# Optimization experiments

Measured on AMD Instinct MI355X. Metric: run time of the kernel, lower is better.

The kernel has to match this reference:

```python
import math
import jax, jax.numpy as jnp
import numpy as np

N_EMBD = 256
N_HEAD = 4
MLP_MULT = 64
N = MLP_MULT * N_EMBD // N_HEAD  # 4096, head feature dim
THETA = 2 ** 16
B, T = 2, 2048


def get_freqs(n: int, theta: int) -> jnp.ndarray:
    # quantize arange to multiples of 2 (pairs share a frequency)
    idx = jnp.arange(n, dtype=jnp.float32)
    q = jnp.floor(idx / 2.0) * 2.0
    return 1.0 / theta ** (q / n) / (2.0 * math.pi)


def _rope(phases: jnp.ndarray, v: jnp.ndarray) -> jnp.ndarray:
    # interleaved rotation: (-v_odd, v_even) re-interleaved
    v_rot = jnp.stack((-v[..., 1::2], v[..., ::2]), axis=-1).reshape(v.shape)
    ph = (phases % 1.0) * (2.0 * math.pi)
    return v * jnp.cos(ph) + v_rot * jnp.sin(ph)


def setup_inputs() -> dict:
    key = jax.random.key(0)
    kq, kk, kv = jax.random.split(key, 3)
    Q = jax.random.normal(kq, (B, N_HEAD, T, N), dtype=jnp.float32)
    K = jax.random.normal(kk, (B, N_HEAD, T, N), dtype=jnp.float32)
    V = jax.random.normal(kv, (B, N_HEAD, T, N), dtype=jnp.float32)
    return {"Q": Q, "K": K, "V": V}


def reference(Q, K, V):
    t = Q.shape[2]
    freqs = get_freqs(N, THETA)  # [N]
    # phases: [1,1,T,N]
    r_phases = jnp.arange(t, dtype=jnp.float32)[None, None, :, None] * freqs[None, None, None, :]
    Q32 = Q.astype(jnp.float32)
    V32 = V.astype(jnp.float32)
    QR = _rope(r_phases, Q32)  # [B,nh,T,N]
    scale = 1.0 / math.sqrt(N)
    scores = jnp.einsum('bhtn,bhsn->bhts', QR, QR) * scale  # [B,nh,T,T], no softmax
    out = jnp.einsum('bhts,bhsn->bhtn', scores, V32)
    return out.astype(Q.dtype)
```

## Files before the change

### kernel.cpp

```cpp
#include <hip/hip_runtime.h>
#include <stdint.h>

#define B_  2
#define H_  4
#define T_  2048
#define N_  4096
#define BH  8

#define BM 256
#define BN 256
#define BK 64

typedef __attribute__((ext_vector_type(8))) short  short8;
typedef __attribute__((ext_vector_type(4))) float  floatx4;


__device__ __forceinline__ unsigned short f2bf(float x) {
  union { float f; unsigned u; } un; un.f = x;
  unsigned r = un.u + 0x7FFFu + ((un.u >> 16) & 1u);
  return (unsigned short)(r >> 16);
}

__device__ __forceinline__ void async_copy16(const void* g, void* l) {
  __builtin_amdgcn_global_load_lds(
      (const __attribute__((address_space(1))) unsigned int*)g,
      (__attribute__((address_space(3))) unsigned int*)l,
      16, 0, 0);
}

__global__ __launch_bounds__(256)
void rope_cast_kernel(const float* __restrict__ Q, unsigned short* __restrict__ QR) {
  const long e0 = ((long)blockIdx.x * 256 + threadIdx.x) * 8;
  const float4 v0 = *(const float4*)(Q + e0);
  const float4 v1 = *(const float4*)(Q + e0 + 4);
  const int   n0 = (int)(e0 & (N_ - 1));
  const float t  = (float)((int)((e0 >> 12) & (T_ - 1)));
  float vv[8] = {v0.x, v0.y, v0.z, v0.w, v1.x, v1.y, v1.z, v1.w};
  union { short8 v; unsigned short u[8]; } o;
#pragma unroll
  for (int p = 0; p < 4; ++p) {
    const int n = n0 + 2 * p;
    const float freq = exp2f(-(float)n * (1.0f / 256.0f)) * 0.15915494309189535f;
    const float ph = t * freq;
    const float fr = ph - floorf(ph);
    const float s = __builtin_amdgcn_sinf(fr);
    const float c = __builtin_amdgcn_cosf(fr);
    o.u[2 * p]     = f2bf(vv[2 * p] * c - vv[2 * p + 1] * s);
    o.u[2 * p + 1] = f2bf(vv[2 * p + 1] * c + vv[2 * p] * s);
  }
  *(short8*)(QR + e0) = o.v;
}

__global__ __launch_bounds__(256)
void transpose_cast_kernel(const float* __restrict__ V, unsigned short* __restrict__ Vt) {
  __shared__ float tile[64][65];
  const long bh = blockIdx.z;
  const float* Vb = V + bh * (long)T_ * N_;
  unsigned short* Vtb = Vt + bh * (long)N_ * T_;
  const int s0 = blockIdx.x * 64;
  const int n0 = blockIdx.y * 64;
  const int tx = threadIdx.x & 63;
  const int ty = threadIdx.x >> 6;
#pragma unroll
  for (int i = 0; i < 16; ++i) {
    const int r = ty * 16 + i;
    tile[r][tx] = Vb[(long)(s0 + r) * N_ + n0 + tx];
  }
  __syncthreads();
#pragma unroll
  for (int i = 0; i < 16; ++i) {
    const int r = ty * 16 + i;
    Vtb[(long)(n0 + r) * T_ + s0 + tx] = f2bf(tile[tx][r]);
  }
}

__device__ __forceinline__ const short8* frag_ptr(const unsigned short* base, int row, int colel) {
  const int half = row >> 7;
  const int r    = row & 127;
  int o = r * 128 + colel * 2;
  o ^= (r & 7) << 4;
  return (const short8*)((const char*)base + half * 16384 + o);
}

__device__ __forceinline__ void load_a8(short8 a[8], const unsigned short* tp, int rb, int lr, int lk) {
#pragma unroll
  for (int f = 0; f < 4; ++f)
#pragma unroll
    for (int s = 0; s < 2; ++s)
      a[f * 2 + s] = *frag_ptr(tp, rb + f * 16 + lr, s * 32 + lk);
}

__device__ __forceinline__ void load_b4(short8 b[4], const unsigned short* tp, int rb, int lr, int lk) {
#pragma unroll
  for (int c = 0; c < 2; ++c)
#pragma unroll
    for (int s = 0; s < 2; ++s)
      b[c * 2 + s] = *frag_ptr(tp, rb + c * 16 + lr, s * 32 + lk);
}

template<int QI, int QJ>
__device__ __forceinline__ void mfma_quad(floatx4 (&acc)[8][4], const short8* a, const short8* b) {
#pragma unroll
  for (int s = 0; s < 2; ++s)
#pragma unroll
    for (int f = 0; f < 4; ++f)
#pragma unroll
      for (int c = 0; c < 2; ++c)
        acc[QI * 4 + f][QJ * 2 + c] = __builtin_amdgcn_mfma_f32_16x16x32_bf16(
            a[f * 2 + s], b[c * 2 + s], acc[QI * 4 + f][QJ * 2 + c], 0, 0, 0);
}

template <typename OutT>
__global__ __launch_bounds__(512, 2)
void gemm_bt8(const unsigned short* __restrict__ A, const unsigned short* __restrict__ B,
              OutT* __restrict__ C, int M, int Nc, int K, float alpha,
              long sA, long sB, long sC)
{
  __shared__ unsigned short smem[4][16384];

  const int nx = (int)gridDim.x, ny = (int)gridDim.y;
  const int nwg = nx * ny * (int)gridDim.z;
  const int idx = (int)blockIdx.x + nx * ((int)blockIdx.y + ny * (int)blockIdx.z);
  const int wg = ((nwg & 7) == 0) ? ((idx & 7) * (nwg >> 3) + (idx >> 3)) : idx;
  const int bx = wg % nx;
  const int by = (wg / nx) % ny;
  const int bz = wg / (nx * ny);

  const unsigned short* Ab = A + bz * sA;
  const unsigned short* Bb = B + bz * sB;
  OutT* Cb = C + bz * sC;
  const int tM = by * BM, tN = bx * BN;

  const int tid  = (int)threadIdx.x;
  const int lane = tid & 63;
  const int wave = tid >> 6;
  const int wm = wave >> 2;
  const int wn = wave & 3;
  const int lr = lane & 15;
  const int lk = (lane >> 4) * 8;

  const int sr = wave * 8 + (lane >> 3);
  const int sc = ((((lane & 7) * 16) ^ ((lane >> 3) << 4)) >> 1);
  const long aoff = (long)(tM + sr) * K + sc;
  const long boff = (long)(tN + sr) * K + sc;
  const int NT = K / BK;

  #define STAGE(Gb, off, kt, h, Lhalf) do {                                        \
    const unsigned short* _g = (Gb) + (off) + (long)(h) * 128 * K + (long)(kt) * 64; \
    async_copy16(_g,                &(Lhalf)[wave * 512]);                          \
    async_copy16(_g + (long)64 * K, &(Lhalf)[4096 + wave * 512]);                   \
  } while (0)

  STAGE(Bb, boff, 0, 0, &smem[1][0]);
  STAGE(Bb, boff, 0, 1, &smem[1][8192]);
  STAGE(Ab, aoff, 0, 0, &smem[0][0]);
  STAGE(Ab, aoff, 0, 1, &smem[0][8192]);
  const int k1 = (NT > 1) ? 1 : 0;
  STAGE(Bb, boff, k1, 0, &smem[3][0]);
  STAGE(Bb, boff, k1, 1, &smem[3][8192]);
  asm volatile("s_waitcnt vmcnt(4)" ::: "memory");
  __builtin_amdgcn_s_barrier();

  floatx4 acc[8][4] = {};
  short8 a[8], b0[4], b1[4];

  for (int t = 0; t < NT; ++t) {
    const unsigned short* Ac = smem[(t & 1) * 2 + 0];
    const unsigned short* Bc = smem[(t & 1) * 2 + 1];
    unsigned short* An = smem[((t + 1) & 1) * 2 + 0];
    unsigned short* Bn = smem[(t & 1) * 2 + 1];
    const int ktA = (t + 1 < NT) ? t + 1 : NT - 1;
    const int ktB = (t + 2 < NT) ? t + 2 : NT - 1;

    load_a8(a,  Ac, wm * 128 + 0,  lr, lk);
    load_b4(b0, Bc, wn * 64 + 0,   lr, lk);
    STAGE(Ab, aoff, ktA, 0, &An[0]);
    __builtin_amdgcn_s_barrier();
    asm volatile("s_waitcnt lgkmcnt(0)" ::: "memory");
    __builtin_amdgcn_s_setprio(1);
    mfma_quad<0, 0>(acc, a, b0);
    __builtin_amdgcn_s_setprio(0);
    __builtin_amdgcn_s_barrier();

    load_b4(b1, Bc, wn * 64 + 32, lr, lk);
    STAGE(Ab, aoff, ktA, 1, &An[8192]);
    __builtin_amdgcn_s_barrier();
    asm volatile("s_waitcnt lgkmcnt(0)" ::: "memory");
    __builtin_amdgcn_s_setprio(1);
    mfma_quad<0, 1>(acc, a, b1);
    __builtin_amdgcn_s_setprio(0);
    __builtin_amdgcn_s_barrier();

    load_a8(a, Ac, wm * 128 + 64, lr, lk);
    STAGE(Bb, boff, ktB, 0, &Bn[0]);
    __builtin_amdgcn_s_barrier();
    asm volatile("s_waitcnt lgkmcnt(0)" ::: "memory");
    __builtin_amdgcn_s_setprio(1);
    mfma_quad<1, 1>(acc, a, b1);
    __builtin_amdgcn_s_setprio(0);
    __builtin_amdgcn_s_barrier();

    STAGE(Bb, boff, ktB, 1, &Bn[8192]);
    asm volatile("s_waitcnt vmcnt(4)" ::: "memory");
    __builtin_amdgcn_s_barrier();
    __builtin_amdgcn_s_setprio(1);
    mfma_quad<1, 0>(acc, a, b0);
    __builtin_amdgcn_s_setprio(0);
    __builtin_amdgcn_s_barrier();
  }
  #undef STAGE

  const int crow = (lane >> 4) * 4;
  const int ccol = lane & 15;
#pragma unroll
  for (int f = 0; f < 8; ++f)
#pragma unroll
    for (int c = 0; c < 4; ++c)
#pragma unroll
      for (int r = 0; r < 4; ++r) {
        const long row = tM + wm * 128 + f * 16 + crow + r;
        const long col = tN + wn * 64 + c * 16 + ccol;
        const float v = acc[f][c][r] * alpha;
        OutT* p = &Cb[row * (long)Nc + col];
        if constexpr (sizeof(OutT) == 2) *p = (OutT)f2bf(v);
        else                             *p = (OutT)v;
      }
}

extern "C" void kernel_launch(void* const* d_in, const int* in_sizes, int n_in,
                              void* d_out, int out_size, void* d_ws, size_t ws_size,
                              hipStream_t stream) {
  const float* Q = (const float*)d_in[0];
  const float* V = (const float*)d_in[2];
  float* O = (float*)d_out;

  unsigned short* QRb = (unsigned short*)d_ws;
  unsigned short* Vtb = QRb + (size_t)BH * T_ * N_;
  unsigned short* S   = Vtb + (size_t)BH * T_ * N_;

  rope_cast_kernel<<<(BH * (long)T_ * N_) / (8 * 256), 256, 0, stream>>>(Q, QRb);
  transpose_cast_kernel<<<dim3(T_ / 64, N_ / 64, BH), 256, 0, stream>>>(V, Vtb);
  gemm_bt8<unsigned short><<<dim3(T_ / BN, T_ / BM, BH), 512, 0, stream>>>(
      QRb, QRb, S, T_, T_, N_, 1.0f / 64.0f,
      (long)T_ * N_, (long)T_ * N_, (long)T_ * T_);
  gemm_bt8<float><<<dim3(N_ / BN, T_ / BM, BH), 512, 0, stream>>>(
      S, Vtb, O, T_, N_, T_, 1.0f,
      (long)T_ * T_, (long)N_ * T_, (long)T_ * N_);
}
```

Before: 1.154 ms.

## Merge rope and transpose prep kernels, vectorize transpose, precompute LDS fragment addresses

Merges the RoPE-cast and V transpose-cast kernels into one launch that picks its role by block index, which removes a kernel launch and lets the two memory-bound passes share the GPU. The transpose now does float4 global reads and 16-byte bf16 writes instead of scalar accesses. The GEMM hoists the swizzled LDS fragment addresses out of the inner loop as per-lane byte offsets with parity toggling, which cuts the integer address math per iteration. Merging the kernels also makes every rope block reserve the transpose tile in shared memory, and the hand-written address math has to match the old swizzle exactly.

```diff
diff --git a/kernel.cpp b/kernel.cpp
--- a/kernel.cpp
+++ b/kernel.cpp
@@ -11,6 +11,9 @@
 #define BN 256
 #define BK 64
 
+#define ROPE_BLOCKS  ((BH * (long)T_ * N_) / (8 * 256))
+#define TRANS_BLOCKS ((T_ / 64) * (N_ / 64) * BH)
+
 typedef __attribute__((ext_vector_type(8))) short  short8;
 typedef __attribute__((ext_vector_type(4))) float  floatx4;
 
@@ -29,73 +32,62 @@
 }
 
 __global__ __launch_bounds__(256)
-void rope_cast_kernel(const float* __restrict__ Q, unsigned short* __restrict__ QR) {
-  const long e0 = ((long)blockIdx.x * 256 + threadIdx.x) * 8;
-  const float4 v0 = *(const float4*)(Q + e0);
-  const float4 v1 = *(const float4*)(Q + e0 + 4);
-  const int   n0 = (int)(e0 & (N_ - 1));
-  const float t  = (float)((int)((e0 >> 12) & (T_ - 1)));
-  float vv[8] = {v0.x, v0.y, v0.z, v0.w, v1.x, v1.y, v1.z, v1.w};
-  union { short8 v; unsigned short u[8]; } o;
-#pragma unroll
-  for (int p = 0; p < 4; ++p) {
-    const int n = n0 + 2 * p;
-    const float freq = exp2f(-(float)n * (1.0f / 256.0f)) * 0.15915494309189535f;
-    const float ph = t * freq;
-    const float fr = ph - floorf(ph);
-    const float s = __builtin_amdgcn_sinf(fr);
-    const float c = __builtin_amdgcn_cosf(fr);
-    o.u[2 * p]     = f2bf(vv[2 * p] * c - vv[2 * p + 1] * s);
-    o.u[2 * p + 1] = f2bf(vv[2 * p + 1] * c + vv[2 * p] * s);
+void prep_kernel(const float* __restrict__ Q, unsigned short* __restrict__ QR,
+                 const float* __restrict__ V, unsigned short* __restrict__ Vt) {
+  __shared__ float tile[64][65];
+  const int bid = (int)blockIdx.x;
+
+  if (bid < (int)ROPE_BLOCKS) {
+    const long e0 = ((long)bid * 256 + threadIdx.x) * 8;
+    const float4 v0 = *(const float4*)(Q + e0);
+    const float4 v1 = *(const float4*)(Q + e0 + 4);
+    const int   n0 = (int)(e0 & (N_ - 1));
+    const float t  = (float)((int)((e0 >> 12) & (T_ - 1)));
+    float vv[8] = {v0.x, v0.y, v0.z, v0.w, v1.x, v1.y, v1.z, v1.w};
+    union { short8 v; unsigned short u[8]; } o;
+#pragma unroll
+    for (int p = 0; p < 4; ++p) {
+      const int n = n0 + 2 * p;
+      const float freq = exp2f(-(float)n * (1.0f / 256.0f)) * 0.15915494309189535f;
+      const float ph = t * freq;
+      const float fr = ph - floorf(ph);
+      const float s = __builtin_amdgcn_sinf(fr);
+      const float c = __builtin_amdgcn_cosf(fr);
+      o.u[2 * p]     = f2bf(vv[2 * p] * c - vv[2 * p + 1] * s);
+      o.u[2 * p + 1] = f2bf(vv[2 * p + 1] * c + vv[2 * p] * s);
+    }
+    *(short8*)(QR + e0) = o.v;
+  } else {
+    const int tb = bid - (int)ROPE_BLOCKS;
+    const int sxi = tb & 31;
+    const int nyi = (tb >> 5) & 63;
+    const long bh = tb >> 11;
+    const float* Vb = V + bh * (long)T_ * N_;
+    unsigned short* Vtb = Vt + bh * (long)N_ * T_;
+    const int s0 = sxi * 64;
+    const int n0 = nyi * 64;
+    const int c = threadIdx.x & 15;
+    const int r = threadIdx.x >> 4;
+#pragma unroll
+    for (int i = 0; i < 4; ++i) {
+      const float4 v = *(const float4*)(Vb + (long)(s0 + r + 16 * i) * N_ + n0 + c * 4);
+      tile[r + 16 * i][c * 4 + 0] = v.x;
+      tile[r + 16 * i][c * 4 + 1] = v.y;
+      tile[r + 16 * i][c * 4 + 2] = v.z;
+      tile[r + 16 * i][c * 4 + 3] = v.w;
+    }
+    __syncthreads();
+    const int rn = threadIdx.x >> 3;
+    const int cs = threadIdx.x & 7;
+#pragma unroll
+    for (int i = 0; i < 2; ++i) {
+      const int n = rn + 32 * i;
+      union { short8 v; unsigned short u[8]; } o;
+#pragma unroll
+      for (int k = 0; k < 8; ++k) o.u[k] = f2bf(tile[cs * 8 + k][n]);
+      *(short8*)(Vtb + (long)(n0 + n) * T_ + s0 + cs * 8) = o.v;
+    }
   }
-  *(short8*)(QR + e0) = o.v;
-}
-
-__global__ __launch_bounds__(256)
-void transpose_cast_kernel(const float* __restrict__ V, unsigned short* __restrict__ Vt) {
-  __shared__ float tile[64][65];
-  const long bh = blockIdx.z;
-  const float* Vb = V + bh * (long)T_ * N_;
-  unsigned short* Vtb = Vt + bh * (long)N_ * T_;
-  const int s0 = blockIdx.x * 64;
-  const int n0 = blockIdx.y * 64;
-  const int tx = threadIdx.x & 63;
-  const int ty = threadIdx.x >> 6;
-#pragma unroll
-  for (int i = 0; i < 16; ++i) {
-    const int r = ty * 16 + i;
-    tile[r][tx] = Vb[(long)(s0 + r) * N_ + n0 + tx];
-  }
-  __syncthreads();
-#pragma unroll
-  for (int i = 0; i < 16; ++i) {
-    const int r = ty * 16 + i;
-    Vtb[(long)(n0 + r) * T_ + s0 + tx] = f2bf(tile[tx][r]);
-  }
-}
-
-__device__ __forceinline__ const short8* frag_ptr(const unsigned short* base, int row, int colel) {
-  const int half = row >> 7;
-  const int r    = row & 127;
-  int o = r * 128 + colel * 2;
-  o ^= (r & 7) << 4;
-  return (const short8*)((const char*)base + half * 16384 + o);
-}
-
-__device__ __forceinline__ void load_a8(short8 a[8], const unsigned short* tp, int rb, int lr, int lk) {
-#pragma unroll
-  for (int f = 0; f < 4; ++f)
-#pragma unroll
-    for (int s = 0; s < 2; ++s)
-      a[f * 2 + s] = *frag_ptr(tp, rb + f * 16 + lr, s * 32 + lk);
-}
-
-__device__ __forceinline__ void load_b4(short8 b[4], const unsigned short* tp, int rb, int lr, int lk) {
-#pragma unroll
-  for (int c = 0; c < 2; ++c)
-#pragma unroll
-    for (int s = 0; s < 2; ++s)
-      b[c * 2 + s] = *frag_ptr(tp, rb + c * 16 + lr, s * 32 + lk);
 }
 
 template<int QI, int QJ>
@@ -117,6 +109,7 @@
               long sA, long sB, long sC)
 {
   __shared__ unsigned short smem[4][16384];
+  char* smemb = (char*)smem;
 
   const int nx = (int)gridDim.x, ny = (int)gridDim.y;
   const int nwg = nx * ny * (int)gridDim.z;
@@ -139,25 +132,32 @@
   const int lr = lane & 15;
   const int lk = (lane >> 4) * 8;
 
+  const unsigned swz   = (unsigned)(lane & 7) << 4;
+  const unsigned lowA0 = ((unsigned)(lk * 2)     ) ^ swz;
+  const unsigned lowA1 = ((unsigned)(lk * 2) + 64) ^ swz;
+  const unsigned aB4   = (unsigned)wm * 16384u + (unsigned)lr * 128u;
+  const unsigned bB4   = 32768u + (unsigned)(wn >> 1) * 16384u
+                       + (unsigned)(wn & 1) * 8192u + (unsigned)lr * 128u;
+
   const int sr = wave * 8 + (lane >> 3);
   const int sc = ((((lane & 7) * 16) ^ ((lane >> 3) << 4)) >> 1);
-  const long aoff = (long)(tM + sr) * K + sc;
-  const long boff = (long)(tN + sr) * K + sc;
+  const unsigned short* gA = Ab + (long)(tM + sr) * K + sc;
+  const unsigned short* gB = Bb + (long)(tN + sr) * K + sc;
   const int NT = K / BK;
 
-  #define STAGE(Gb, off, kt, h, Lhalf) do {                                        \
-    const unsigned short* _g = (Gb) + (off) + (long)(h) * 128 * K + (long)(kt) * 64; \
-    async_copy16(_g,                &(Lhalf)[wave * 512]);                          \
-    async_copy16(_g + (long)64 * K, &(Lhalf)[4096 + wave * 512]);                   \
+  #define STAGE2(gbase, kt, h, ldst) do {                                          \
+    const unsigned short* _g = (gbase) + (long)(kt) * 64 + (long)((h) * 128) * K;  \
+    async_copy16(_g,                (char*)(ldst) + wave * 1024);                  \
+    async_copy16(_g + (long)64 * K, (char*)(ldst) + 8192 + wave * 1024);           \
   } while (0)
 
-  STAGE(Bb, boff, 0, 0, &smem[1][0]);
-  STAGE(Bb, boff, 0, 1, &smem[1][8192]);
-  STAGE(Ab, aoff, 0, 0, &smem[0][0]);
-  STAGE(Ab, aoff, 0, 1, &smem[0][8192]);
+  STAGE2(gB, 0, 0, smemb + 32768);
+  STAGE2(gB, 0, 1, smemb + 32768 + 16384);
+  STAGE2(gA, 0, 0, smemb + 0);
+  STAGE2(gA, 0, 1, smemb + 16384);
   const int k1 = (NT > 1) ? 1 : 0;
-  STAGE(Bb, boff, k1, 0, &smem[3][0]);
-  STAGE(Bb, boff, k1, 1, &smem[3][8192]);
+  STAGE2(gB, k1, 0, smemb + 65536 + 32768);
+  STAGE2(gB, k1, 1, smemb + 65536 + 32768 + 16384);
   asm volatile("s_waitcnt vmcnt(4)" ::: "memory");
   __builtin_amdgcn_s_barrier();
 
@@ -165,16 +165,26 @@
   short8 a[8], b0[4], b1[4];
 
   for (int t = 0; t < NT; ++t) {
-    const unsigned short* Ac = smem[(t & 1) * 2 + 0];
-    const unsigned short* Bc = smem[(t & 1) * 2 + 1];
-    unsigned short* An = smem[((t + 1) & 1) * 2 + 0];
-    unsigned short* Bn = smem[(t & 1) * 2 + 1];
+    const unsigned par  = (unsigned)(t & 1) << 16;
+    const unsigned parn = par ^ 0x10000u;
+    const char* pa0 = smemb + (par + aB4 + lowA0);
+    const char* pa1 = smemb + (par + aB4 + lowA1);
+    const char* pb0 = smemb + (par + bB4 + lowA0);
+    const char* pb1 = smemb + (par + bB4 + lowA1);
     const int ktA = (t + 1 < NT) ? t + 1 : NT - 1;
     const int ktB = (t + 2 < NT) ? t + 2 : NT - 1;
 
-    load_a8(a,  Ac, wm * 128 + 0,  lr, lk);
-    load_b4(b0, Bc, wn * 64 + 0,   lr, lk);
-    STAGE(Ab, aoff, ktA, 0, &An[0]);
+#pragma unroll
+    for (int f = 0; f < 4; ++f) {
+      a[f * 2 + 0] = *(const short8*)(pa0 + f * 2048);
+      a[f * 2 + 1] = *(const short8*)(pa1 + f * 2048);
+    }
+#pragma unroll
+    for (int c = 0; c < 2; ++c) {
+      b0[c * 2 + 0] = *(const short8*)(pb0 + c * 2048);
+      b0[c * 2 + 1] = *(const short8*)(pb1 + c * 2048);
+    }
+    STAGE2(gA, ktA, 0, smemb + parn);
     __builtin_amdgcn_s_barrier();
     asm volatile("s_waitcnt lgkmcnt(0)" ::: "memory");
     __builtin_amdgcn_s_setprio(1);
@@ -182,8 +192,12 @@
     __builtin_amdgcn_s_setprio(0);
     __builtin_amdgcn_s_barrier();
 
-    load_b4(b1, Bc, wn * 64 + 32, lr, lk);
-    STAGE(Ab, aoff, ktA, 1, &An[8192]);
+#pragma unroll
+    for (int c = 0; c < 2; ++c) {
+      b1[c * 2 + 0] = *(const short8*)(pb0 + 4096 + c * 2048);
+      b1[c * 2 + 1] = *(const short8*)(pb1 + 4096 + c * 2048);
+    }
+    STAGE2(gA, ktA, 1, smemb + parn + 16384);
     __builtin_amdgcn_s_barrier();
     asm volatile("s_waitcnt lgkmcnt(0)" ::: "memory");
     __builtin_amdgcn_s_setprio(1);
@@ -191,8 +205,12 @@
     __builtin_amdgcn_s_setprio(0);
     __builtin_amdgcn_s_barrier();
 
-    load_a8(a, Ac, wm * 128 + 64, lr, lk);
-    STAGE(Bb, boff, ktB, 0, &Bn[0]);
+#pragma unroll
+    for (int f = 0; f < 4; ++f) {
+      a[f * 2 + 0] = *(const short8*)(pa0 + 8192 + f * 2048);
+      a[f * 2 + 1] = *(const short8*)(pa1 + 8192 + f * 2048);
+    }
+    STAGE2(gB, ktB, 0, smemb + par + 32768);
     __builtin_amdgcn_s_barrier();
     asm volatile("s_waitcnt lgkmcnt(0)" ::: "memory");
     __builtin_amdgcn_s_setprio(1);
@@ -200,7 +218,7 @@
     __builtin_amdgcn_s_setprio(0);
     __builtin_amdgcn_s_barrier();
 
-    STAGE(Bb, boff, ktB, 1, &Bn[8192]);
+    STAGE2(gB, ktB, 1, smemb + par + 32768 + 16384);
     asm volatile("s_waitcnt vmcnt(4)" ::: "memory");
     __builtin_amdgcn_s_barrier();
     __builtin_amdgcn_s_setprio(1);
@@ -208,7 +226,7 @@
     __builtin_amdgcn_s_setprio(0);
     __builtin_amdgcn_s_barrier();
   }
-  #undef STAGE
+  #undef STAGE2
 
   const int crow = (lane >> 4) * 4;
   const int ccol = lane & 15;
@@ -238,8 +256,7 @@
   unsigned short* Vtb = QRb + (size_t)BH * T_ * N_;
   unsigned short* S   = Vtb + (size_t)BH * T_ * N_;
 
-  rope_cast_kernel<<<(BH * (long)T_ * N_) / (8 * 256), 256, 0, stream>>>(Q, QRb);
-  transpose_cast_kernel<<<dim3(T_ / 64, N_ / 64, BH), 256, 0, stream>>>(V, Vtb);
+  prep_kernel<<<(int)(ROPE_BLOCKS + TRANS_BLOCKS), 256, 0, stream>>>(Q, QRb, V, Vtb);
   gemm_bt8<unsigned short><<<dim3(T_ / BN, T_ / BM, BH), 512, 0, stream>>>(
       QRb, QRb, S, T_, T_, N_, 1.0f / 64.0f,
       (long)T_ * N_, (long)T_ * N_, (long)T_ * T_);
```

New measurement: 1.151 ms. No clear change (-0.3%).
